# Performance work log

Hardware: AMD Instinct MI355X
Metric: run time of the kernel (lower is better)

The kernel has to match this reference:

```python
import jax, jax.numpy as jnp
import numpy as np

NUM_E = 100000
NUM_REL2 = 460  # 2 * num_rel
H = 200
N_EDGES = 1000000
B = 512
RRELU_SLOPE = (1.0 / 8.0 + 1.0 / 3.0) / 2.0  # F.rrelu eval-mode slope
BN_EPS = 1e-5


def setup_inputs() -> dict:
    key = jax.random.key(0)
    ks = jax.random.split(key, 20)
    d = {}
    d["ent_emb"] = jax.random.normal(ks[0], (NUM_E, H), jnp.float32) * 0.1
    d["rel_emb"] = jax.random.normal(ks[1], (NUM_REL2, H), jnp.float32) * 0.1
    d["W_neigh1"] = jax.random.normal(ks[2], (H, H), jnp.float32) * (1.0 / np.sqrt(H))
    d["W_loop1"] = jax.random.normal(ks[3], (H, H), jnp.float32) * (1.0 / np.sqrt(H))
    d["W_neigh2"] = jax.random.normal(ks[4], (H, H), jnp.float32) * (1.0 / np.sqrt(H))
    d["W_loop2"] = jax.random.normal(ks[5], (H, H), jnp.float32) * (1.0 / np.sqrt(H))
    d["gate_theta"] = jax.random.normal(ks[6], (NUM_E, H), jnp.float32) * 0.1
    d["gate_w"] = jax.random.normal(ks[7], (H, 1), jnp.float32) * (1.0 / np.sqrt(H))
    d["gate_b"] = jnp.zeros((1,), jnp.float32)
    d["bn_gamma"] = jnp.ones((3,), jnp.float32)
    d["bn_beta"] = jnp.zeros((3,), jnp.float32)
    d["conv_w"] = jax.random.normal(ks[8], (3,), jnp.float32)
    d["conv_b"] = jnp.zeros((1,), jnp.float32)
    d["freq"] = jax.random.normal(ks[9], (B, H), jnp.float32)
    d["src"] = jax.random.randint(ks[10], (N_EDGES,), 0, NUM_E, jnp.int64)
    d["dst"] = jax.random.randint(ks[11], (N_EDGES,), 0, NUM_E, jnp.int64)
    d["etype"] = jax.random.randint(ks[12], (N_EDGES,), 0, NUM_REL2, jnp.int64)
    d["s_idx"] = jax.random.randint(ks[13], (B,), 0, NUM_E, jnp.int64)
    d["r_idx"] = jax.random.randint(ks[14], (B,), 0, NUM_REL2, jnp.int64)
    return d


def _rrelu(x):
    return jnp.where(x >= 0, x, x * RRELU_SLOPE)


def _union_rgcn_layer(h, rel, W_neigh, W_loop, src, dst):
    # gather -> transform -> scatter (UnionRGCNLayer msg: (h_src + r_etype) @ W_neigh)
    msg = (h[src] + rel) @ W_neigh                      # [E, H]
    agg = jax.ops.segment_sum(msg, dst, num_segments=NUM_E)
    deg = jax.ops.segment_sum(jnp.ones((msg.shape[0],), h.dtype), dst, num_segments=NUM_E)
    agg = agg / jnp.maximum(deg, 1.0)[:, None]          # in-degree norm
    return _rrelu(agg + h @ W_loop)                     # self-loop + activation (dropout off, eval)


def reference(ent_emb, rel_emb, W_neigh1, W_loop1, W_neigh2, W_loop2,
              gate_theta, gate_w, gate_b, bn_gamma, bn_beta, conv_w, conv_b,
              freq, src, dst, etype, s_idx, r_idx):
    rel_per_edge = rel_emb[etype]                       # [E, H]
    # RGCNCell: 2 UnionRGCN layers
    h = _union_rgcn_layer(ent_emb, rel_per_edge, W_neigh1, W_loop1, src, dst)
    h = _union_rgcn_layer(h, rel_per_edge, W_neigh2, W_loop2, src, dst)
    # GatingMechanism: gate = sigmoid(linear(gate_theta[ids])); blend evolved vs static
    gate = jax.nn.sigmoid(gate_theta @ gate_w + gate_b)  # [N, 1]
    h_final = gate * h + (1.0 - gate) * ent_emb          # [N, H]
    # ConvE fusion: stack (entity, rel, frequency) as 3 channels
    e = h_final[s_idx]                                   # [B, H]
    r = rel_emb[r_idx]                                   # [B, H]
    x = jnp.stack([e, r, freq], axis=1)                  # [B, 3, H]
    # BatchNorm1d(3), batch statistics over (B, H) per channel
    mean = jnp.mean(x, axis=(0, 2), keepdims=True)
    var = jnp.var(x, axis=(0, 2), keepdims=True)
    x = (x - mean) * jax.lax.rsqrt(var + BN_EPS)
    x = x * bn_gamma[None, :, None] + bn_beta[None, :, None]
    x = jax.nn.relu(x)
    # Conv1d(3 -> 1, kernel_size=1): weighted channel sum
    q = jnp.einsum('bch,c->bh', x, conv_w) + conv_b      # [B, H]
    # score against all (evolved) entity embeddings
    scores = q @ h_final.T                               # [B, N]
    return scores
```

## Files before the change

### kernel.cpp

```cpp
#include <hip/hip_runtime.h>

#define N_ENT 100000
#define HDIM  200
#define NEDGE 1000000
#define BDIM  512
#define PITCH 224
#define NSEG  28
#define NF    13
#define SCAN_TILE 1024
#define SCAN_NB   ((N_ENT + SCAN_TILE - 1)/SCAN_TILE)
#define BN_NB 32
#define RELB_ELEMS (460*PITCH)
#define BP_ELEMS   (14*NF*64*8)

typedef short  short8v __attribute__((ext_vector_type(8)));
typedef float  float4v __attribute__((ext_vector_type(4)));

__device__ __forceinline__ float rrelu_f(float v){
    const float slope = (1.0f/8.0f + 1.0f/3.0f)*0.5f;
    return v >= 0.f ? v : v*slope;
}
__device__ __forceinline__ unsigned short f2bf(float f){
    unsigned int x = __float_as_uint(f);
    unsigned int r = (x + 0x7fffu + ((x >> 16) & 1u)) >> 16;
    return (unsigned short)r;
}
__device__ __forceinline__ float bf2f(unsigned short u){
    return __uint_as_float(((unsigned int)u) << 16);
}

__device__ __forceinline__ void pack_b(int b, const float* __restrict__ Wn,
        const float* __restrict__ Wl, unsigned short* __restrict__ Bp){
    int i = b*1024 + threadIdx.x*4;
    #pragma unroll
    for (int k=0;k<4;k++){
        int idx = i+k;
        if (idx < BP_ELEMS){
            int j = idx & 7, l = (idx >> 3) & 63, rest = idx >> 9;
            int f = rest % NF, ks = rest / NF;
            int kk = ks*32 + ((l >> 4) << 3) + j;
            int c  = f*16 + (l & 15);
            float v = 0.f;
            if (c < HDIM){
                if (kk < 200)                  v = Wn[(size_t)kk*HDIM + c];
                else if (kk >= 224 && kk < 424) v = Wl[(size_t)(kk-224)*HDIM + c];
            }
            Bp[idx] = f2bf(v);
        }
    }
}

__global__ __launch_bounds__(256) void init_k(const float* __restrict__ ent,
        const float* __restrict__ rel,
        const float* __restrict__ Wn1, const float* __restrict__ Wl1,
        const float* __restrict__ Wn2, const float* __restrict__ Wl2,
        int* __restrict__ deg, unsigned short* __restrict__ relb,
        unsigned short* __restrict__ Bp1, unsigned short* __restrict__ Bp2,
        unsigned short* __restrict__ Xbuf1){
    int b = blockIdx.x;
    if (b < 98){
        int i = b*1024 + threadIdx.x*4;
        if (i+3 < N_ENT) *(int4*)(deg+i) = make_int4(0,0,0,0);
        else { for (int k=0;k<4;k++) if (i+k < N_ENT) deg[i+k]=0; }
        return;
    }
    b -= 98;
    if (b < 101){
        int i = b*1024 + threadIdx.x*4;
        #pragma unroll
        for (int k=0;k<4;k++){
            int idx = i+k;
            if (idx < RELB_ELEMS){
                int r = idx / PITCH, c = idx - r*PITCH;
                relb[idx] = (c < HDIM) ? f2bf(rel[(size_t)r*HDIM + c]) : 0;
            }
        }
        return;
    }
    b -= 101;
    if (b < 91){ pack_b(b, Wn1, Wl1, Bp1); return; }
    b -= 91;
    if (b < 91){ pack_b(b, Wn2, Wl2, Bp2); return; }
    b -= 91;
    int w = threadIdx.x >> 6, l = threadIdx.x & 63;
    if (l >= 56) return;
    int n = b*4 + w;
    int el = 4*l;
    ushort4 o;
    if (el < HDIM){
        float4 v = *(const float4*)(ent + (size_t)n*HDIM + el);
        o.x=f2bf(v.x); o.y=f2bf(v.y); o.z=f2bf(v.z); o.w=f2bf(v.w);
    } else {
        o.x=o.y=o.z=o.w=0;
    }
    *(ushort4*)(Xbuf1 + (size_t)n*PITCH + el) = o;
}

__global__ void hist_k(const int* __restrict__ dst, int* __restrict__ deg){
    int e = blockIdx.x*blockDim.x + threadIdx.x;
    if (e < NEDGE) atomicAdd(&deg[dst[e]], 1);
}

__global__ __launch_bounds__(256) void scan_part_k(const int* __restrict__ deg, int* __restrict__ partial){
    int t = threadIdx.x;
    int base = blockIdx.x*SCAN_TILE + t*4;
    int s = 0;
    if (base + 3 < N_ENT){
        int4 v = *(const int4*)(deg + base);
        s = v.x + v.y + v.z + v.w;
    } else {
        for (int i=0;i<4;i++) if (base+i < N_ENT) s += deg[base+i];
    }
    #pragma unroll
    for (int off=32; off>=1; off>>=1) s += __shfl_xor(s, off);
    __shared__ int ws[4];
    if ((t&63)==0) ws[t>>6] = s;
    __syncthreads();
    if (t==0) partial[blockIdx.x] = ws[0]+ws[1]+ws[2]+ws[3];
}

__global__ void scan_mid_k(int* __restrict__ partial){
    __shared__ int sh[128];
    int t = threadIdx.x;
    int v = (t < SCAN_NB) ? partial[t] : 0;
    sh[t] = v;
    __syncthreads();
    for (int off=1; off<128; off<<=1){
        int u = (t>=off) ? sh[t-off] : 0;
        __syncthreads();
        sh[t] += u;
        __syncthreads();
    }
    if (t < SCAN_NB) partial[t] = sh[t] - v;
}

__global__ __launch_bounds__(256) void scan_fin_k(const int* __restrict__ deg, const int* __restrict__ partial,
        int* __restrict__ row_off, int* __restrict__ fill_pos){
    int t = threadIdx.x;
    int lane = t & 63;
    int base = blockIdx.x*SCAN_TILE + t*4;
    int v0=0,v1=0,v2=0,v3=0;
    if (base+3 < N_ENT){
        int4 v = *(const int4*)(deg + base);
        v0=v.x; v1=v.y; v2=v.z; v3=v.w;
    } else {
        if (base   < N_ENT) v0 = deg[base];
        if (base+1 < N_ENT) v1 = deg[base+1];
        if (base+2 < N_ENT) v2 = deg[base+2];
        if (base+3 < N_ENT) v3 = deg[base+3];
    }
    int s = v0+v1+v2+v3;
    int inc = s;
    #pragma unroll
    for (int off=1; off<64; off<<=1){
        int u = __shfl_up(inc, off);
        if (lane >= off) inc += u;
    }
    __shared__ int wsum[4];
    if (lane==63) wsum[t>>6] = inc;
    __syncthreads();
    int w = t>>6;
    int woff = 0;
    for (int i=0;i<w;i++) woff += wsum[i];
    int exc = partial[blockIdx.x] + woff + inc - s;
    int r0 = exc, r1 = exc+v0, r2 = exc+v0+v1, r3 = exc+v0+v1+v2;
    if (base+3 < N_ENT){
        *(int4*)(row_off+base)  = make_int4(r0,r1,r2,r3);
        *(int4*)(fill_pos+base) = make_int4(r0,r1,r2,r3);
    } else {
        if (base   < N_ENT){ row_off[base]  =r0; fill_pos[base]  =r0; }
        if (base+1 < N_ENT){ row_off[base+1]=r1; fill_pos[base+1]=r1; }
        if (base+2 < N_ENT){ row_off[base+2]=r2; fill_pos[base+2]=r2; }
        if (base+3 < N_ENT){ row_off[base+3]=r3; fill_pos[base+3]=r3; }
    }
    if (blockIdx.x==0 && t==0) row_off[N_ENT] = NEDGE;
}

__global__ void fill_k(const int* __restrict__ src, const int* __restrict__ dst, const int* __restrict__ et,
                       int* __restrict__ fill_pos, int2* __restrict__ cs){
    int e = blockIdx.x*blockDim.x + threadIdx.x;
    if (e < NEDGE){
        int p = atomicAdd(&fill_pos[dst[e]], 1);
        cs[p] = make_int2(src[e], et[e]);
    }
}

__global__ __launch_bounds__(256) void spmm1_k(const unsigned short* __restrict__ X,
        unsigned short* __restrict__ P,
        const unsigned short* __restrict__ relb,
        const int2* __restrict__ cs,
        const int* __restrict__ row_off,
        unsigned short* __restrict__ relavg){
    int wv = (blockIdx.x*256 + threadIdx.x) >> 6;
    int l = threadIdx.x & 63;
    if (l >= 56) return;
    int beg = row_off[wv], end = row_off[wv+1];
    const int el = 4*l;
    float x0=0.f,x1=0.f,x2=0.f,x3=0.f;
    float r0=0.f,r1=0.f,r2=0.f,r3=0.f;
    int e = beg;
    for (; e+4 <= end; e+=4){
        int2 c0 = cs[e], c1 = cs[e+1], c2 = cs[e+2], c3 = cs[e+3];
        ushort4 xa = *(const ushort4*)(X + (size_t)c0.x*PITCH + el);
        ushort4 xb = *(const ushort4*)(X + (size_t)c1.x*PITCH + el);
        ushort4 xc = *(const ushort4*)(X + (size_t)c2.x*PITCH + el);
        ushort4 xd = *(const ushort4*)(X + (size_t)c3.x*PITCH + el);
        ushort4 ra = *(const ushort4*)(relb + (size_t)c0.y*PITCH + el);
        ushort4 rb = *(const ushort4*)(relb + (size_t)c1.y*PITCH + el);
        ushort4 rc = *(const ushort4*)(relb + (size_t)c2.y*PITCH + el);
        ushort4 rd = *(const ushort4*)(relb + (size_t)c3.y*PITCH + el);
        x0 += bf2f(xa.x)+bf2f(xb.x)+bf2f(xc.x)+bf2f(xd.x);
        x1 += bf2f(xa.y)+bf2f(xb.y)+bf2f(xc.y)+bf2f(xd.y);
        x2 += bf2f(xa.z)+bf2f(xb.z)+bf2f(xc.z)+bf2f(xd.z);
        x3 += bf2f(xa.w)+bf2f(xb.w)+bf2f(xc.w)+bf2f(xd.w);
        r0 += bf2f(ra.x)+bf2f(rb.x)+bf2f(rc.x)+bf2f(rd.x);
        r1 += bf2f(ra.y)+bf2f(rb.y)+bf2f(rc.y)+bf2f(rd.y);
        r2 += bf2f(ra.z)+bf2f(rb.z)+bf2f(rc.z)+bf2f(rd.z);
        r3 += bf2f(ra.w)+bf2f(rb.w)+bf2f(rc.w)+bf2f(rd.w);
    }
    for (; e<end; e++){
        int2 c0 = cs[e];
        ushort4 xa = *(const ushort4*)(X + (size_t)c0.x*PITCH + el);
        ushort4 ra = *(const ushort4*)(relb + (size_t)c0.y*PITCH + el);
        x0 += bf2f(xa.x); x1 += bf2f(xa.y); x2 += bf2f(xa.z); x3 += bf2f(xa.w);
        r0 += bf2f(ra.x); r1 += bf2f(ra.y); r2 += bf2f(ra.z); r3 += bf2f(ra.w);
    }
    float id = 1.f / fmaxf((float)(end-beg), 1.f);
    float g0 = r0*id, g1 = r1*id, g2 = r2*id, g3 = r3*id;
    ushort4 rv; rv.x=f2bf(g0); rv.y=f2bf(g1); rv.z=f2bf(g2); rv.w=f2bf(g3);
    *(ushort4*)(relavg + (size_t)wv*PITCH + el) = rv;
    ushort4 o;
    o.x=f2bf(x0*id+g0); o.y=f2bf(x1*id+g1); o.z=f2bf(x2*id+g2); o.w=f2bf(x3*id+g3);
    *(ushort4*)(P + (size_t)wv*PITCH + el) = o;
}

__global__ __launch_bounds__(256) void spmm2_k(const unsigned short* __restrict__ X,
        unsigned short* __restrict__ P,
        const unsigned short* __restrict__ relavg,
        const int2* __restrict__ cs,
        const int* __restrict__ row_off){
    int wv = (blockIdx.x*256 + threadIdx.x) >> 6;
    int l = threadIdx.x & 63;
    if (l >= 56) return;
    int beg = row_off[wv], end = row_off[wv+1];
    const int el = 4*l;
    float x0=0.f,x1=0.f,x2=0.f,x3=0.f;
    int e = beg;
    for (; e+4 <= end; e+=4){
        int2 c0 = cs[e], c1 = cs[e+1], c2 = cs[e+2], c3 = cs[e+3];
        ushort4 xa = *(const ushort4*)(X + (size_t)c0.x*PITCH + el);
        ushort4 xb = *(const ushort4*)(X + (size_t)c1.x*PITCH + el);
        ushort4 xc = *(const ushort4*)(X + (size_t)c2.x*PITCH + el);
        ushort4 xd = *(const ushort4*)(X + (size_t)c3.x*PITCH + el);
        x0 += bf2f(xa.x)+bf2f(xb.x)+bf2f(xc.x)+bf2f(xd.x);
        x1 += bf2f(xa.y)+bf2f(xb.y)+bf2f(xc.y)+bf2f(xd.y);
        x2 += bf2f(xa.z)+bf2f(xb.z)+bf2f(xc.z)+bf2f(xd.z);
        x3 += bf2f(xa.w)+bf2f(xb.w)+bf2f(xc.w)+bf2f(xd.w);
    }
    for (; e<end; e++){
        int2 c0 = cs[e];
        ushort4 xa = *(const ushort4*)(X + (size_t)c0.x*PITCH + el);
        x0 += bf2f(xa.x); x1 += bf2f(xa.y); x2 += bf2f(xa.z); x3 += bf2f(xa.w);
    }
    float id = 1.f / fmaxf((float)(end-beg), 1.f);
    ushort4 rv = *(const ushort4*)(relavg + (size_t)wv*PITCH + el);
    ushort4 o;
    o.x=f2bf(x0*id+bf2f(rv.x)); o.y=f2bf(x1*id+bf2f(rv.y));
    o.z=f2bf(x2*id+bf2f(rv.z)); o.w=f2bf(x3*id+bf2f(rv.w));
    *(ushort4*)(P + (size_t)wv*PITCH + el) = o;
}

__global__ __launch_bounds__(256) void gate_k(const float* __restrict__ th, const float* __restrict__ gw,
                       const float* __restrict__ gb, float* __restrict__ gate){
    int wv = (blockIdx.x*256 + threadIdx.x)>>6;
    int lane = threadIdx.x & 63;
    const float* t = th + (size_t)wv*HDIM;
    float s = t[lane]*gw[lane] + t[64+lane]*gw[64+lane] + t[128+lane]*gw[128+lane];
    if (lane<8) s += t[192+lane]*gw[192+lane];
    #pragma unroll
    for (int off=32; off>=1; off>>=1) s += __shfl_xor(s, off);
    if (lane==0) gate[wv] = 1.f/(1.f + expf(-(s + gb[0])));
}

template<int EPI>
__global__ __launch_bounds__(256,2) void gemm_layer_mfma_k(
        const unsigned short* __restrict__ Pb,
        const unsigned short* __restrict__ Xb,
        const unsigned short* __restrict__ Bpack,
        unsigned short* __restrict__ OutB,
        const float* __restrict__ gate, const float* __restrict__ ent){
    __shared__ unsigned short OutS[128*PITCH];
    const int tid = threadIdx.x;
    const int l   = tid & 63;
    const int w   = tid >> 6;
    const int n0  = blockIdx.x * 128;
    const int lr  = l & 15;
    const int lg  = l >> 4;
    int r0 = n0 + w*32 + lr;
    int r1 = r0 + 16;
    int c0 = r0 < N_ENT ? r0 : N_ENT-1;
    int c1 = r1 < N_ENT ? r1 : N_ENT-1;
    float4v acc[2][NF];
    #pragma unroll
    for (int f=0; f<NF; f++){
        acc[0][f] = (float4v){0.f,0.f,0.f,0.f};
        acc[1][f] = (float4v){0.f,0.f,0.f,0.f};
    }
    #pragma unroll 1
    for (int sec=0; sec<2; sec++){
        const unsigned short* base = sec ? Xb : Pb;
        const unsigned short* a0p = base + (size_t)c0*PITCH + lg*8;
        const unsigned short* a1p = base + (size_t)c1*PITCH + lg*8;
        const unsigned short* bp0 = Bpack + (((size_t)(sec*7*NF))*64 + l)*8;
        for (int ks=0; ks<7; ks++){
            short8v a0 = *(const short8v*)(a0p + ks*32);
            short8v a1 = *(const short8v*)(a1p + ks*32);
            const unsigned short* bp = bp0 + (size_t)ks*NF*512;
            #pragma unroll
            for (int f=0; f<NF; f++){
                short8v b = *(const short8v*)(bp + (size_t)f*512);
                acc[0][f] = __builtin_amdgcn_mfma_f32_16x16x32_bf16(a0, b, acc[0][f], 0, 0, 0);
                acc[1][f] = __builtin_amdgcn_mfma_f32_16x16x32_bf16(a1, b, acc[1][f], 0, 0, 0);
            }
        }
    }
    #pragma unroll
    for (int f=0; f<NF; f++){
        int c = f*16 + lr;
        if (c < HDIM){
            #pragma unroll
            for (int j=0; j<4; j++){
                OutS[(w*32 + lg*4 + j)*PITCH + c]      = f2bf(rrelu_f(acc[0][f][j]));
                OutS[(w*32 + 16 + lg*4 + j)*PITCH + c] = f2bf(rrelu_f(acc[1][f][j]));
            }
        }
    }
    __syncthreads();
    for (int i = tid; i < 128*NSEG; i += 256){
        int r = i/NSEG, seg = i - r*NSEG;
        int n = n0 + r;
        if (n >= N_ENT) continue;
        short8v o;
        if (seg >= 25){
            #pragma unroll
            for (int j=0;j<8;j++) o[j]=0;
        } else {
            short8v v = *(const short8v*)(&OutS[r*PITCH + seg*8]);
            if (EPI == 2){
                float g = gate[n];
                const float4* ef = (const float4*)(ent + (size_t)n*HDIM + seg*8);
                float4 e0 = ef[0], e1 = ef[1];
                float ev[8] = {e0.x,e0.y,e0.z,e0.w,e1.x,e1.y,e1.z,e1.w};
                #pragma unroll
                for (int j=0; j<8; j++){
                    float x = g*bf2f((unsigned short)v[j]) + (1.f-g)*ev[j];
                    o[j] = (short)f2bf(x);
                }
            } else {
                o = v;
            }
        }
        *(short8v*)(OutB + (size_t)n*PITCH + seg*8) = o;
    }
}

__global__ __launch_bounds__(256) void bn_part_k(const unsigned short* __restrict__ hfb,
        const float* __restrict__ rel, const float* __restrict__ freq,
        const int* __restrict__ s_idx, const int* __restrict__ r_idx,
        float* __restrict__ bnpart){
    int t = threadIdx.x;
    float acc[6] = {0,0,0,0,0,0};
    for (int i = blockIdx.x*256 + t; i < BDIM*HDIM; i += BN_NB*256){
        int b = i/HDIM, h = i - b*HDIM;
        float e = bf2f(hfb[(size_t)s_idx[b]*PITCH + h]);
        float r = rel[(size_t)r_idx[b]*HDIM + h];
        float f = freq[i];
        acc[0]+=e; acc[1]+=e*e; acc[2]+=r; acc[3]+=r*r; acc[4]+=f; acc[5]+=f*f;
    }
    __shared__ float red[4][6];
    #pragma unroll
    for (int c=0;c<6;c++){
        float s = acc[c];
        #pragma unroll
        for (int off=32; off>=1; off>>=1) s += __shfl_xor(s, off);
        if ((t&63)==0) red[t>>6][c] = s;
    }
    __syncthreads();
    if (t==0){
        #pragma unroll
        for (int c=0;c<6;c++)
            bnpart[blockIdx.x*6+c] = red[0][c]+red[1][c]+red[2][c]+red[3][c];
    }
}

__global__ void bn_fin_k(const float* __restrict__ bnpart, float* __restrict__ bnp){
    int t = threadIdx.x;
    if (t < 3){
        float s=0.f, q=0.f;
        for (int b=0;b<BN_NB;b++){ s += bnpart[b*6+2*t]; q += bnpart[b*6+2*t+1]; }
        const float inv = 1.f/(float)(BDIM*HDIM);
        float mean = s*inv;
        float var  = q*inv - mean*mean;
        bnp[t]   = mean;
        bnp[3+t] = rsqrtf(var + 1e-5f);
    }
}

__global__ void qt_k(const unsigned short* __restrict__ hfb, const float* __restrict__ rel,
        const float* __restrict__ freq, const int* __restrict__ s_idx, const int* __restrict__ r_idx,
        const float* __restrict__ gamma, const float* __restrict__ beta,
        const float* __restrict__ convw, const float* __restrict__ convb,
        const float* __restrict__ bnp, unsigned short* __restrict__ qb){
    int i = blockIdx.x*blockDim.x + threadIdx.x;
    if (i >= BDIM*PITCH) return;
    int b = i/PITCH, h = i - b*PITCH;
    if (h >= HDIM){ qb[i] = 0; return; }
    float x0 = bf2f(hfb[(size_t)s_idx[b]*PITCH + h]);
    float x1 = rel[(size_t)r_idx[b]*HDIM + h];
    float x2 = freq[(size_t)b*HDIM + h];
    float v0 = fmaxf((x0-bnp[0])*bnp[3]*gamma[0] + beta[0], 0.f);
    float v1 = fmaxf((x1-bnp[1])*bnp[4]*gamma[1] + beta[1], 0.f);
    float v2 = fmaxf((x2-bnp[2])*bnp[5]*gamma[2] + beta[2], 0.f);
    float q = v0*convw[0] + v1*convw[1] + v2*convw[2] + convb[0];
    qb[(size_t)b*PITCH + h] = f2bf(q);
}

__global__ __launch_bounds__(256,2) void scores_mfma_k(
        const unsigned short* __restrict__ hfb,
        const unsigned short* __restrict__ qb,
        float* __restrict__ out){
    const int tid = threadIdx.x;
    const int l   = tid & 63;
    const int w   = tid >> 6;
    const int lr  = l & 15;
    const int lg  = l >> 4;
    const int n0  = blockIdx.x * 64;
    float4v acc[8][4];
    #pragma unroll
    for (int bf=0; bf<8; bf++)
        #pragma unroll
        for (int nf=0; nf<4; nf++) acc[bf][nf] = (float4v){0,0,0,0};
    const unsigned short* hptr[4];
    #pragma unroll
    for (int nf=0; nf<4; nf++){
        int n = n0 + nf*16 + lr;
        if (n >= N_ENT) n = N_ENT-1;
        hptr[nf] = hfb + (size_t)n*PITCH + lg*8;
    }
    const unsigned short* qrow = qb + (size_t)(w*128 + lr)*PITCH + lg*8;
    for (int ks=0; ks<7; ks++){
        short8v hv[4];
        #pragma unroll
        for (int nf=0; nf<4; nf++) hv[nf] = *(const short8v*)(hptr[nf] + ks*32);
        #pragma unroll
        for (int bf=0; bf<8; bf++){
            short8v q = *(const short8v*)(qrow + (size_t)bf*16*PITCH + ks*32);
            #pragma unroll
            for (int nf=0; nf<4; nf++)
                acc[bf][nf] = __builtin_amdgcn_mfma_f32_16x16x32_bf16(q, hv[nf], acc[bf][nf], 0, 0, 0);
        }
    }
    #pragma unroll
    for (int bf=0; bf<8; bf++){
        int b = w*128 + bf*16 + lg*4;
        #pragma unroll
        for (int nf=0; nf<4; nf++){
            int n = n0 + nf*16 + lr;
            if (n >= N_ENT) continue;
            #pragma unroll
            for (int j=0; j<4; j++){
                out[(size_t)(b+j)*N_ENT + n] = acc[bf][nf][j];
            }
        }
    }
}

extern "C" void kernel_launch(void* const* d_in, const int* in_sizes, int n_in,
                              void* d_out, int out_size, void* d_ws, size_t ws_size,
                              hipStream_t stream) {
    const float* ent    = (const float*)d_in[0];
    const float* rel    = (const float*)d_in[1];
    const float* Wn1    = (const float*)d_in[2];
    const float* Wl1    = (const float*)d_in[3];
    const float* Wn2    = (const float*)d_in[4];
    const float* Wl2    = (const float*)d_in[5];
    const float* gtheta = (const float*)d_in[6];
    const float* gw     = (const float*)d_in[7];
    const float* gb     = (const float*)d_in[8];
    const float* gamma  = (const float*)d_in[9];
    const float* beta   = (const float*)d_in[10];
    const float* convw  = (const float*)d_in[11];
    const float* convb  = (const float*)d_in[12];
    const float* freq   = (const float*)d_in[13];
    const int*   src    = (const int*)d_in[14];
    const int*   dst    = (const int*)d_in[15];
    const int*   etype  = (const int*)d_in[16];
    const int*   s_idx  = (const int*)d_in[17];
    const int*   r_idx  = (const int*)d_in[18];
    float* out = (float*)d_out;

    char* ws = (char*)d_ws;
    size_t off = 0;
    auto alloc = [&](size_t bytes)->char*{
        char* p = ws + off;
        off += (bytes + 511) & ~(size_t)511;
        return p;
    };
    int*   deg      = (int*)alloc((size_t)N_ENT*4);
    int*   row_off  = (int*)alloc((size_t)(N_ENT+1)*4);
    int*   fill_pos = (int*)alloc((size_t)N_ENT*4);
    int*   partial  = (int*)alloc((size_t)SCAN_NB*4);
    int2*  cs       = (int2*)alloc((size_t)NEDGE*8);
    unsigned short* Xbuf1  = (unsigned short*)alloc((size_t)N_ENT*PITCH*2);
    unsigned short* Pbuf1  = (unsigned short*)alloc((size_t)N_ENT*PITCH*2);
    unsigned short* Xbuf2  = (unsigned short*)alloc((size_t)N_ENT*PITCH*2);
    unsigned short* Pbuf2  = (unsigned short*)alloc((size_t)N_ENT*PITCH*2);
    unsigned short* relavg = (unsigned short*)alloc((size_t)N_ENT*PITCH*2);
    unsigned short* relb   = (unsigned short*)alloc((size_t)RELB_ELEMS*2);
    unsigned short* Bp1    = (unsigned short*)alloc((size_t)BP_ELEMS*2);
    unsigned short* Bp2    = (unsigned short*)alloc((size_t)BP_ELEMS*2);
    unsigned short* qb     = (unsigned short*)alloc((size_t)BDIM*PITCH*2);
    float* gate   = (float*)alloc((size_t)N_ENT*4);
    float* bnpart = (float*)alloc((size_t)BN_NB*6*4);
    float* bnp    = (float*)alloc(64);
    unsigned short* hfb = Xbuf1;

    const int EB = (NEDGE + 255)/256;
    const int INIT_NB = 98 + 101 + 91 + 91 + N_ENT/4;

    init_k<<<INIT_NB,256,0,stream>>>(ent, rel, Wn1, Wl1, Wn2, Wl2, deg, relb, Bp1, Bp2, Xbuf1);
    hist_k<<<EB,256,0,stream>>>(dst, deg);
    scan_part_k<<<SCAN_NB,256,0,stream>>>(deg, partial);
    scan_mid_k<<<1,128,0,stream>>>(partial);
    scan_fin_k<<<SCAN_NB,256,0,stream>>>(deg, partial, row_off, fill_pos);
    fill_k<<<EB,256,0,stream>>>(src, dst, etype, fill_pos, cs);
    gate_k<<<N_ENT/4,256,0,stream>>>(gtheta, gw, gb, gate);

    const int NWB = N_ENT/4;
    const int GTB = (N_ENT + 127)/128;

    spmm1_k<<<NWB,256,0,stream>>>(Xbuf1, Pbuf1, relb, cs, row_off, relavg);
    gemm_layer_mfma_k<1><<<GTB,256,0,stream>>>(Pbuf1, Xbuf1, Bp1, Xbuf2, nullptr, nullptr);

    spmm2_k<<<NWB,256,0,stream>>>(Xbuf2, Pbuf2, relavg, cs, row_off);
    gemm_layer_mfma_k<2><<<GTB,256,0,stream>>>(Pbuf2, Xbuf2, Bp2, hfb, gate, ent);

    bn_part_k<<<BN_NB,256,0,stream>>>(hfb, rel, freq, s_idx, r_idx, bnpart);
    bn_fin_k<<<1,64,0,stream>>>(bnpart, bnp);
    qt_k<<<(BDIM*PITCH+255)/256,256,0,stream>>>(hfb, rel, freq, s_idx, r_idx, gamma, beta, convw, convb, bnp, qb);

    scores_mfma_k<<<(N_ENT+63)/64,256,0,stream>>>(hfb, qb, out);

    (void)in_sizes; (void)n_in; (void)out_size; (void)ws_size;
}
```

Baseline: 574.3 us.

## Gather neighbor features in FP8 copies and fold gate and BN-finalize kernels

Each layer's input now also gets an FP8 copy: init_k writes it for layer 1 and the layer-1 GEMM epilogue writes it for layer 2. Both SpMM gathers read 4-byte FP8 words in place of 8-byte bf16 words, which roughly halves the random-access traffic of the edge gather. The gate computation moves into the init kernel and the BN finalize step moves into qt_k, removing two launches. The cost is extra FP8 writes and lower precision in the neighbor aggregation, which may affect accuracy.

```diff
diff --git a/kernel.cpp b/kernel.cpp
--- a/kernel.cpp
+++ b/kernel.cpp
@@ -5,6 +5,7 @@
 #define NEDGE 1000000
 #define BDIM  512
 #define PITCH 224
+#define PITCH8 256
 #define NSEG  28
 #define NF    13
 #define SCAN_TILE 1024
@@ -15,6 +16,7 @@
 
 typedef short  short8v __attribute__((ext_vector_type(8)));
 typedef float  float4v __attribute__((ext_vector_type(4)));
+typedef float  float2v __attribute__((ext_vector_type(2)));
 
 __device__ __forceinline__ float rrelu_f(float v){
     const float slope = (1.0f/8.0f + 1.0f/3.0f)*0.5f;
@@ -27,6 +29,12 @@
 }
 __device__ __forceinline__ float bf2f(unsigned short u){
     return __uint_as_float(((unsigned int)u) << 16);
+}
+__device__ __forceinline__ unsigned int pack_fp8x4(float a, float b, float c, float d){
+    unsigned int w = 0;
+    w = __builtin_amdgcn_cvt_pk_fp8_f32(a, b, w, false);
+    w = __builtin_amdgcn_cvt_pk_fp8_f32(c, d, w, true);
+    return w;
 }
 
 __device__ __forceinline__ void pack_b(int b, const float* __restrict__ Wn,
@@ -42,7 +50,7 @@
             int c  = f*16 + (l & 15);
             float v = 0.f;
             if (c < HDIM){
-                if (kk < 200)                  v = Wn[(size_t)kk*HDIM + c];
+                if (kk < 200)                   v = Wn[(size_t)kk*HDIM + c];
                 else if (kk >= 224 && kk < 424) v = Wl[(size_t)(kk-224)*HDIM + c];
             }
             Bp[idx] = f2bf(v);
@@ -54,9 +62,12 @@
         const float* __restrict__ rel,
         const float* __restrict__ Wn1, const float* __restrict__ Wl1,
         const float* __restrict__ Wn2, const float* __restrict__ Wl2,
+        const float* __restrict__ gtheta, const float* __restrict__ gw,
+        const float* __restrict__ gb,
         int* __restrict__ deg, unsigned short* __restrict__ relb,
         unsigned short* __restrict__ Bp1, unsigned short* __restrict__ Bp2,
-        unsigned short* __restrict__ Xbuf1){
+        unsigned short* __restrict__ Xbuf1, unsigned char* __restrict__ X8_1,
+        float* __restrict__ gate){
     int b = blockIdx.x;
     if (b < 98){
         int i = b*1024 + threadIdx.x*4;
@@ -83,17 +94,28 @@
     if (b < 91){ pack_b(b, Wn2, Wl2, Bp2); return; }
     b -= 91;
     int w = threadIdx.x >> 6, l = threadIdx.x & 63;
-    if (l >= 56) return;
-    int n = b*4 + w;
-    int el = 4*l;
-    ushort4 o;
-    if (el < HDIM){
-        float4 v = *(const float4*)(ent + (size_t)n*HDIM + el);
+    if (b < N_ENT/4){
+        if (l >= 56) return;
+        int n = b*4 + w;
+        int el = 4*l;
+        ushort4 o;
+        float4 v = make_float4(0.f,0.f,0.f,0.f);
+        if (el < HDIM) v = *(const float4*)(ent + (size_t)n*HDIM + el);
         o.x=f2bf(v.x); o.y=f2bf(v.y); o.z=f2bf(v.z); o.w=f2bf(v.w);
-    } else {
-        o.x=o.y=o.z=o.w=0;
-    }
-    *(ushort4*)(Xbuf1 + (size_t)n*PITCH + el) = o;
+        *(ushort4*)(Xbuf1 + (size_t)n*PITCH + el) = o;
+        *(unsigned int*)(X8_1 + (size_t)n*PITCH8 + el) = pack_fp8x4(v.x,v.y,v.z,v.w);
+        return;
+    }
+    b -= N_ENT/4;
+    {
+        int n = b*4 + w;
+        const float* t = gtheta + (size_t)n*HDIM;
+        float s = t[l]*gw[l] + t[64+l]*gw[64+l] + t[128+l]*gw[128+l];
+        if (l<8) s += t[192+l]*gw[192+l];
+        #pragma unroll
+        for (int off=32; off>=1; off>>=1) s += __shfl_xor(s, off);
+        if (l==0) gate[n] = 1.f/(1.f + expf(-(s + gb[0])));
+    }
 }
 
 __global__ void hist_k(const int* __restrict__ dst, int* __restrict__ deg){
@@ -185,7 +207,7 @@
     }
 }
 
-__global__ __launch_bounds__(256) void spmm1_k(const unsigned short* __restrict__ X,
+__global__ __launch_bounds__(256) void spmm1_k(const unsigned char* __restrict__ X8,
         unsigned short* __restrict__ P,
         const unsigned short* __restrict__ relb,
         const int2* __restrict__ cs,
@@ -201,18 +223,26 @@
     int e = beg;
     for (; e+4 <= end; e+=4){
         int2 c0 = cs[e], c1 = cs[e+1], c2 = cs[e+2], c3 = cs[e+3];
-        ushort4 xa = *(const ushort4*)(X + (size_t)c0.x*PITCH + el);
-        ushort4 xb = *(const ushort4*)(X + (size_t)c1.x*PITCH + el);
-        ushort4 xc = *(const ushort4*)(X + (size_t)c2.x*PITCH + el);
-        ushort4 xd = *(const ushort4*)(X + (size_t)c3.x*PITCH + el);
+        unsigned int ua = *(const unsigned int*)(X8 + (size_t)c0.x*PITCH8 + el);
+        unsigned int ub = *(const unsigned int*)(X8 + (size_t)c1.x*PITCH8 + el);
+        unsigned int uc = *(const unsigned int*)(X8 + (size_t)c2.x*PITCH8 + el);
+        unsigned int ud = *(const unsigned int*)(X8 + (size_t)c3.x*PITCH8 + el);
         ushort4 ra = *(const ushort4*)(relb + (size_t)c0.y*PITCH + el);
         ushort4 rb = *(const ushort4*)(relb + (size_t)c1.y*PITCH + el);
         ushort4 rc = *(const ushort4*)(relb + (size_t)c2.y*PITCH + el);
         ushort4 rd = *(const ushort4*)(relb + (size_t)c3.y*PITCH + el);
-        x0 += bf2f(xa.x)+bf2f(xb.x)+bf2f(xc.x)+bf2f(xd.x);
-        x1 += bf2f(xa.y)+bf2f(xb.y)+bf2f(xc.y)+bf2f(xd.y);
-        x2 += bf2f(xa.z)+bf2f(xb.z)+bf2f(xc.z)+bf2f(xd.z);
-        x3 += bf2f(xa.w)+bf2f(xb.w)+bf2f(xc.w)+bf2f(xd.w);
+        float2v alo = __builtin_amdgcn_cvt_pk_f32_fp8((int)ua, false);
+        float2v ahi = __builtin_amdgcn_cvt_pk_f32_fp8((int)ua, true);
+        float2v blo = __builtin_amdgcn_cvt_pk_f32_fp8((int)ub, false);
+        float2v bhi = __builtin_amdgcn_cvt_pk_f32_fp8((int)ub, true);
+        float2v clo = __builtin_amdgcn_cvt_pk_f32_fp8((int)uc, false);
+        float2v chi = __builtin_amdgcn_cvt_pk_f32_fp8((int)uc, true);
+        float2v dlo = __builtin_amdgcn_cvt_pk_f32_fp8((int)ud, false);
+        float2v dhi = __builtin_amdgcn_cvt_pk_f32_fp8((int)ud, true);
+        x0 += alo[0]+blo[0]+clo[0]+dlo[0];
+        x1 += alo[1]+blo[1]+clo[1]+dlo[1];
+        x2 += ahi[0]+bhi[0]+chi[0]+dhi[0];
+        x3 += ahi[1]+bhi[1]+chi[1]+dhi[1];
         r0 += bf2f(ra.x)+bf2f(rb.x)+bf2f(rc.x)+bf2f(rd.x);
         r1 += bf2f(ra.y)+bf2f(rb.y)+bf2f(rc.y)+bf2f(rd.y);
         r2 += bf2f(ra.z)+bf2f(rb.z)+bf2f(rc.z)+bf2f(rd.z);
@@ -220,9 +250,11 @@
     }
     for (; e<end; e++){
         int2 c0 = cs[e];
-        ushort4 xa = *(const ushort4*)(X + (size_t)c0.x*PITCH + el);
+        unsigned int ua = *(const unsigned int*)(X8 + (size_t)c0.x*PITCH8 + el);
         ushort4 ra = *(const ushort4*)(relb + (size_t)c0.y*PITCH + el);
-        x0 += bf2f(xa.x); x1 += bf2f(xa.y); x2 += bf2f(xa.z); x3 += bf2f(xa.w);
+        float2v alo = __builtin_amdgcn_cvt_pk_f32_fp8((int)ua, false);
+        float2v ahi = __builtin_amdgcn_cvt_pk_f32_fp8((int)ua, true);
+        x0 += alo[0]; x1 += alo[1]; x2 += ahi[0]; x3 += ahi[1];
         r0 += bf2f(ra.x); r1 += bf2f(ra.y); r2 += bf2f(ra.z); r3 += bf2f(ra.w);
     }
     float id = 1.f / fmaxf((float)(end-beg), 1.f);
@@ -234,7 +266,7 @@
     *(ushort4*)(P + (size_t)wv*PITCH + el) = o;
 }
 
-__global__ __launch_bounds__(256) void spmm2_k(const unsigned short* __restrict__ X,
+__global__ __launch_bounds__(256) void spmm2_k(const unsigned char* __restrict__ X8,
         unsigned short* __restrict__ P,
         const unsigned short* __restrict__ relavg,
         const int2* __restrict__ cs,
@@ -244,42 +276,40 @@
     if (l >= 56) return;
     int beg = row_off[wv], end = row_off[wv+1];
     const int el = 4*l;
+    ushort4 rv = *(const ushort4*)(relavg + (size_t)wv*PITCH + el);
     float x0=0.f,x1=0.f,x2=0.f,x3=0.f;
     int e = beg;
     for (; e+4 <= end; e+=4){
         int2 c0 = cs[e], c1 = cs[e+1], c2 = cs[e+2], c3 = cs[e+3];
-        ushort4 xa = *(const ushort4*)(X + (size_t)c0.x*PITCH + el);
-        ushort4 xb = *(const ushort4*)(X + (size_t)c1.x*PITCH + el);
-        ushort4 xc = *(const ushort4*)(X + (size_t)c2.x*PITCH + el);
-        ushort4 xd = *(const ushort4*)(X + (size_t)c3.x*PITCH + el);
-        x0 += bf2f(xa.x)+bf2f(xb.x)+bf2f(xc.x)+bf2f(xd.x);
-        x1 += bf2f(xa.y)+bf2f(xb.y)+bf2f(xc.y)+bf2f(xd.y);
-        x2 += bf2f(xa.z)+bf2f(xb.z)+bf2f(xc.z)+bf2f(xd.z);
-        x3 += bf2f(xa.w)+bf2f(xb.w)+bf2f(xc.w)+bf2f(xd.w);
+        unsigned int ua = *(const unsigned int*)(X8 + (size_t)c0.x*PITCH8 + el);
+        unsigned int ub = *(const unsigned int*)(X8 + (size_t)c1.x*PITCH8 + el);
+        unsigned int uc = *(const unsigned int*)(X8 + (size_t)c2.x*PITCH8 + el);
+        unsigned int ud = *(const unsigned int*)(X8 + (size_t)c3.x*PITCH8 + el);
+        float2v alo = __builtin_amdgcn_cvt_pk_f32_fp8((int)ua, false);
+        float2v ahi = __builtin_amdgcn_cvt_pk_f32_fp8((int)ua, true);
+        float2v blo = __builtin_amdgcn_cvt_pk_f32_fp8((int)ub, false);
+        float2v bhi = __builtin_amdgcn_cvt_pk_f32_fp8((int)ub, true);
+        float2v clo = __builtin_amdgcn_cvt_pk_f32_fp8((int)uc, false);
+        float2v chi = __builtin_amdgcn_cvt_pk_f32_fp8((int)uc, true);
+        float2v dlo = __builtin_amdgcn_cvt_pk_f32_fp8((int)ud, false);
+        float2v dhi = __builtin_amdgcn_cvt_pk_f32_fp8((int)ud, true);
+        x0 += alo[0]+blo[0]+clo[0]+dlo[0];
+        x1 += alo[1]+blo[1]+clo[1]+dlo[1];
+        x2 += ahi[0]+bhi[0]+chi[0]+dhi[0];
+        x3 += ahi[1]+bhi[1]+chi[1]+dhi[1];
     }
     for (; e<end; e++){
         int2 c0 = cs[e];
-        ushort4 xa = *(const ushort4*)(X + (size_t)c0.x*PITCH + el);
-        x0 += bf2f(xa.x); x1 += bf2f(xa.y); x2 += bf2f(xa.z); x3 += bf2f(xa.w);
+        unsigned int ua = *(const unsigned int*)(X8 + (size_t)c0.x*PITCH8 + el);
+        float2v alo = __builtin_amdgcn_cvt_pk_f32_fp8((int)ua, false);
+        float2v ahi = __builtin_amdgcn_cvt_pk_f32_fp8((int)ua, true);
+        x0 += alo[0]; x1 += alo[1]; x2 += ahi[0]; x3 += ahi[1];
     }
     float id = 1.f / fmaxf((float)(end-beg), 1.f);
-    ushort4 rv = *(const ushort4*)(relavg + (size_t)wv*PITCH + el);
     ushort4 o;
     o.x=f2bf(x0*id+bf2f(rv.x)); o.y=f2bf(x1*id+bf2f(rv.y));
     o.z=f2bf(x2*id+bf2f(rv.z)); o.w=f2bf(x3*id+bf2f(rv.w));
     *(ushort4*)(P + (size_t)wv*PITCH + el) = o;
-}
-
-__global__ __launch_bounds__(256) void gate_k(const float* __restrict__ th, const float* __restrict__ gw,
-                       const float* __restrict__ gb, float* __restrict__ gate){
-    int wv = (blockIdx.x*256 + threadIdx.x)>>6;
-    int lane = threadIdx.x & 63;
-    const float* t = th + (size_t)wv*HDIM;
-    float s = t[lane]*gw[lane] + t[64+lane]*gw[64+lane] + t[128+lane]*gw[128+lane];
-    if (lane<8) s += t[192+lane]*gw[192+lane];
-    #pragma unroll
-    for (int off=32; off>=1; off>>=1) s += __shfl_xor(s, off);
-    if (lane==0) gate[wv] = 1.f/(1.f + expf(-(s + gb[0])));
 }
 
 template<int EPI>
@@ -288,6 +318,7 @@
         const unsigned short* __restrict__ Xb,
         const unsigned short* __restrict__ Bpack,
         unsigned short* __restrict__ OutB,
+        unsigned char* __restrict__ X8out,
         const float* __restrict__ gate, const float* __restrict__ ent){
     __shared__ unsigned short OutS[128*PITCH];
     const int tid = threadIdx.x;
@@ -341,6 +372,7 @@
         int n = n0 + r;
         if (n >= N_ENT) continue;
         short8v o;
+        uint2 p8 = make_uint2(0u, 0u);
         if (seg >= 25){
             #pragma unroll
             for (int j=0;j<8;j++) o[j]=0;
@@ -358,9 +390,16 @@
                 }
             } else {
                 o = v;
+                float f0=bf2f((unsigned short)v[0]), f1=bf2f((unsigned short)v[1]);
+                float f2=bf2f((unsigned short)v[2]), f3=bf2f((unsigned short)v[3]);
+                float f4=bf2f((unsigned short)v[4]), f5=bf2f((unsigned short)v[5]);
+                float f6=bf2f((unsigned short)v[6]), f7=bf2f((unsigned short)v[7]);
+                p8.x = pack_fp8x4(f0,f1,f2,f3);
+                p8.y = pack_fp8x4(f4,f5,f6,f7);
             }
         }
         *(short8v*)(OutB + (size_t)n*PITCH + seg*8) = o;
+        if (EPI == 1) *(uint2*)(X8out + (size_t)n*PITCH8 + seg*8) = p8;
     }
 }
 
@@ -393,24 +432,24 @@
     }
 }
 
-__global__ void bn_fin_k(const float* __restrict__ bnpart, float* __restrict__ bnp){
-    int t = threadIdx.x;
-    if (t < 3){
-        float s=0.f, q=0.f;
-        for (int b=0;b<BN_NB;b++){ s += bnpart[b*6+2*t]; q += bnpart[b*6+2*t+1]; }
-        const float inv = 1.f/(float)(BDIM*HDIM);
-        float mean = s*inv;
-        float var  = q*inv - mean*mean;
-        bnp[t]   = mean;
-        bnp[3+t] = rsqrtf(var + 1e-5f);
-    }
-}
-
-__global__ void qt_k(const unsigned short* __restrict__ hfb, const float* __restrict__ rel,
+__global__ __launch_bounds__(256) void qt_k(const unsigned short* __restrict__ hfb,
+        const float* __restrict__ rel,
         const float* __restrict__ freq, const int* __restrict__ s_idx, const int* __restrict__ r_idx,
         const float* __restrict__ gamma, const float* __restrict__ beta,
         const float* __restrict__ convw, const float* __restrict__ convb,
-        const float* __restrict__ bnp, unsigned short* __restrict__ qb){
+        const float* __restrict__ bnpart, unsigned short* __restrict__ qb){
+    __shared__ float bnp_s[6];
+    if (threadIdx.x < 6){
+        float s = 0.f;
+        for (int b=0;b<BN_NB;b++) s += bnpart[b*6 + threadIdx.x];
+        bnp_s[threadIdx.x] = s;
+    }
+    __syncthreads();
+    const float inv = 1.f/(float)(BDIM*HDIM);
+    float m0 = bnp_s[0]*inv, m1 = bnp_s[2]*inv, m2 = bnp_s[4]*inv;
+    float i0 = rsqrtf(bnp_s[1]*inv - m0*m0 + 1e-5f);
+    float i1 = rsqrtf(bnp_s[3]*inv - m1*m1 + 1e-5f);
+    float i2 = rsqrtf(bnp_s[5]*inv - m2*m2 + 1e-5f);
     int i = blockIdx.x*blockDim.x + threadIdx.x;
     if (i >= BDIM*PITCH) return;
     int b = i/PITCH, h = i - b*PITCH;
@@ -418,9 +457,9 @@
     float x0 = bf2f(hfb[(size_t)s_idx[b]*PITCH + h]);
     float x1 = rel[(size_t)r_idx[b]*HDIM + h];
     float x2 = freq[(size_t)b*HDIM + h];
-    float v0 = fmaxf((x0-bnp[0])*bnp[3]*gamma[0] + beta[0], 0.f);
-    float v1 = fmaxf((x1-bnp[1])*bnp[4]*gamma[1] + beta[1], 0.f);
-    float v2 = fmaxf((x2-bnp[2])*bnp[5]*gamma[2] + beta[2], 0.f);
+    float v0 = fmaxf((x0-m0)*i0*gamma[0] + beta[0], 0.f);
+    float v1 = fmaxf((x1-m1)*i1*gamma[1] + beta[1], 0.f);
+    float v2 = fmaxf((x2-m2)*i2*gamma[2] + beta[2], 0.f);
     float q = v0*convw[0] + v1*convw[1] + v2*convw[2] + convb[0];
     qb[(size_t)b*PITCH + h] = f2bf(q);
 }
@@ -512,42 +551,41 @@
     int*   partial  = (int*)alloc((size_t)SCAN_NB*4);
     int2*  cs       = (int2*)alloc((size_t)NEDGE*8);
     unsigned short* Xbuf1  = (unsigned short*)alloc((size_t)N_ENT*PITCH*2);
-    unsigned short* Pbuf1  = (unsigned short*)alloc((size_t)N_ENT*PITCH*2);
     unsigned short* Xbuf2  = (unsigned short*)alloc((size_t)N_ENT*PITCH*2);
-    unsigned short* Pbuf2  = (unsigned short*)alloc((size_t)N_ENT*PITCH*2);
+    unsigned short* Pbuf   = (unsigned short*)alloc((size_t)N_ENT*PITCH*2);
     unsigned short* relavg = (unsigned short*)alloc((size_t)N_ENT*PITCH*2);
+    unsigned char*  X8_1   = (unsigned char*)alloc((size_t)N_ENT*PITCH8);
+    unsigned char*  X8_2   = (unsigned char*)alloc((size_t)N_ENT*PITCH8);
     unsigned short* relb   = (unsigned short*)alloc((size_t)RELB_ELEMS*2);
     unsigned short* Bp1    = (unsigned short*)alloc((size_t)BP_ELEMS*2);
     unsigned short* Bp2    = (unsigned short*)alloc((size_t)BP_ELEMS*2);
     unsigned short* qb     = (unsigned short*)alloc((size_t)BDIM*PITCH*2);
     float* gate   = (float*)alloc((size_t)N_ENT*4);
     float* bnpart = (float*)alloc((size_t)BN_NB*6*4);
-    float* bnp    = (float*)alloc(64);
     unsigned short* hfb = Xbuf1;
 
     const int EB = (NEDGE + 255)/256;
-    const int INIT_NB = 98 + 101 + 91 + 91 + N_ENT/4;
-
-    init_k<<<INIT_NB,256,0,stream>>>(ent, rel, Wn1, Wl1, Wn2, Wl2, deg, relb, Bp1, Bp2, Xbuf1);
+    const int INIT_NB = 98 + 101 + 91 + 91 + N_ENT/4 + N_ENT/4;
+
+    init_k<<<INIT_NB,256,0,stream>>>(ent, rel, Wn1, Wl1, Wn2, Wl2, gtheta, gw, gb,
+                                     deg, relb, Bp1, Bp2, Xbuf1, X8_1, gate);
     hist_k<<<EB,256,0,stream>>>(dst, deg);
     scan_part_k<<<SCAN_NB,256,0,stream>>>(deg, partial);
     scan_mid_k<<<1,128,0,stream>>>(partial);
     scan_fin_k<<<SCAN_NB,256,0,stream>>>(deg, partial, row_off, fill_pos);
     fill_k<<<EB,256,0,stream>>>(src, dst, etype, fill_pos, cs);
-    gate_k<<<N_ENT/4,256,0,stream>>>(gtheta, gw, gb, gate);
 
     const int NWB = N_ENT/4;
     const int GTB = (N_ENT + 127)/128;
 
-    spmm1_k<<<NWB,256,0,stream>>>(Xbuf1, Pbuf1, relb, cs, row_off, relavg);
-    gemm_layer_mfma_k<1><<<GTB,256,0,stream>>>(Pbuf1, Xbuf1, Bp1, Xbuf2, nullptr, nullptr);
-
-    spmm2_k<<<NWB,256,0,stream>>>(Xbuf2, Pbuf2, relavg, cs, row_off);
-    gemm_layer_mfma_k<2><<<GTB,256,0,stream>>>(Pbuf2, Xbuf2, Bp2, hfb, gate, ent);
+    spmm1_k<<<NWB,256,0,stream>>>(X8_1, Pbuf, relb, cs, row_off, relavg);
+    gemm_layer_mfma_k<1><<<GTB,256,0,stream>>>(Pbuf, Xbuf1, Bp1, Xbuf2, X8_2, nullptr, nullptr);
+
+    spmm2_k<<<NWB,256,0,stream>>>(X8_2, Pbuf, relavg, cs, row_off);
+    gemm_layer_mfma_k<2><<<GTB,256,0,stream>>>(Pbuf, Xbuf2, Bp2, hfb, nullptr, gate, ent);
 
     bn_part_k<<<BN_NB,256,0,stream>>>(hfb, rel, freq, s_idx, r_idx, bnpart);
-    bn_fin_k<<<1,64,0,stream>>>(bnpart, bnp);
-    qt_k<<<(BDIM*PITCH+255)/256,256,0,stream>>>(hfb, rel, freq, s_idx, r_idx, gamma, beta, convw, convb, bnp, qb);
+    qt_k<<<(BDIM*PITCH+255)/256,256,0,stream>>>(hfb, rel, freq, s_idx, r_idx, gamma, beta, convw, convb, bnpart, qb);
 
     scores_mfma_k<<<(N_ENT+63)/64,256,0,stream>>>(hfb, qb, out);
 
```

Result: no change. 563.6 us (-1.9%).
